# Optimization experiments

Hardware: AMD Instinct MI355X
Metric: run time of the kernel (lower is better)

## Reference

```python
import jax, jax.numpy as jnp
import numpy as np

N_NODES = 100000
N_EDGES = 1600000
D_IN = 128
D_OUT = 128


def setup_inputs() -> dict:
    key = jax.random.key(0)
    k_x, k_s, k_r, k_w = jax.random.split(key, 4)
    x = jax.random.normal(k_x, (N_NODES, D_IN), dtype=jnp.float32)
    senders = jax.random.randint(k_s, (N_EDGES,), 0, N_NODES, dtype=jnp.int32)
    receivers = jax.random.randint(k_r, (N_EDGES,), 0, N_NODES, dtype=jnp.int32)
    # xavier_uniform for (D_IN, D_OUT)
    limit = float(np.sqrt(6.0 / (D_IN + D_OUT)))
    weight = jax.random.uniform(k_w, (D_IN, D_OUT), dtype=jnp.float32,
                                minval=-limit, maxval=limit)
    bias = jnp.zeros((D_OUT,), dtype=jnp.float32)
    return {"x": x, "senders": senders, "receivers": receivers,
            "n_node": N_NODES, "weight": weight, "bias": bias}


def reference(x, senders, receivers, n_node, weight, bias):
    # Linear node update: [N, D_in] @ [D_in, D_out] + bias
    h = jnp.dot(x, weight) + bias
    total_num_nodes = x.shape[0]

    # Degree counts via segment_sum of ones (symmetric normalization)
    ones = jnp.ones_like(senders)
    sender_degree = jax.ops.segment_sum(ones, senders, num_segments=total_num_nodes)
    receiver_degree = jax.ops.segment_sum(ones, receivers, num_segments=total_num_nodes)

    # Pre-scale by 1/sqrt(deg_out), scatter-sum along edges, post-scale by 1/sqrt(deg_in)
    h = h * jax.lax.rsqrt(jnp.maximum(sender_degree, 1.0))[:, None]
    agg = jax.ops.segment_sum(h[senders], receivers, num_segments=total_num_nodes)
    out = agg * jax.lax.rsqrt(jnp.maximum(receiver_degree, 1.0))[:, None]
    return out
```

## Files before the change

kernel.cpp:

```cpp
#include <hip/hip_runtime.h>
#include <hip/hip_bf16.h>
#include <stdint.h>

#define N_NODES 100000
#define N_EDGES 1600000
#define TILE 8192
#define NB 196
#define BIN_BLOCKS ((N_EDGES + TILE - 1) / TILE)

static const size_t OFF_H      = 0;
static const size_t OFF_SSCALE = 25600000;
static const size_t OFF_ROWP   = 26000000;
static const size_t OFF_RHIST  = 26400016;
static const size_t OFF_SHIST  = 26401040;
static const size_t OFF_RBASE  = 26402064;
static const size_t OFF_SBASE  = 26403088;
static const size_t OFF_RCUR   = 26404112;
static const size_t OFF_SCUR   = 26405136;
static const size_t OFF_WFRAG  = 26406160;
static const size_t OFF_EBUF   = 26438928;
static const size_t OFF_SBUF   = 32838928;

using short8 = __attribute__((ext_vector_type(8))) short;
using f32x4  = __attribute__((ext_vector_type(4))) float;

static __device__ __forceinline__ short f2bf(float f) {
    uint32_t u = __float_as_uint(f);
    uint32_t r = (u + 0x7fffu + ((u >> 16) & 1u)) >> 16;
    return (short)r;
}

__global__ __launch_bounds__(256) void prep_w_kernel(const float* __restrict__ W,
                                                     short8* __restrict__ wfrag) {
    int slot = blockIdx.x * 256 + threadIdx.x;
    int f = slot >> 6, lane = slot & 63;
    int quad = lane >> 4, mcol = lane & 15;
    int s = f >> 3, c = f & 7;
    int krow = s * 32 + quad * 8;
    int ncol = c * 16 + mcol;
    short8 wf;
    #pragma unroll
    for (int j = 0; j < 8; j++)
        wf[j] = f2bf(W[(krow + j) * 128 + ncol]);
    wfrag[slot] = wf;
}

__global__ __launch_bounds__(256) void hist196_kernel(const int* __restrict__ snd,
                                                      const int* __restrict__ rcv,
                                                      int* __restrict__ rhist,
                                                      int* __restrict__ shist) {
    __shared__ int hr[256], hs[256];
    int t = threadIdx.x;
    hr[t] = 0; hs[t] = 0;
    __syncthreads();
    int base = blockIdx.x * TILE;
    #pragma unroll
    for (int j = 0; j < 32; j++) {
        int idx = base + j * 256 + t;
        if (idx < N_EDGES) {
            atomicAdd(&hr[rcv[idx] >> 9], 1);
            atomicAdd(&hs[snd[idx] >> 9], 1);
        }
    }
    __syncthreads();
    if (t < NB) {
        if (hr[t]) atomicAdd(&rhist[t], hr[t]);
        if (hs[t]) atomicAdd(&shist[t], hs[t]);
    }
}

__global__ __launch_bounds__(256) void scanb_kernel(const int* __restrict__ rhist,
                                                    const int* __restrict__ shist,
                                                    int* __restrict__ rbase,
                                                    int* __restrict__ sbase,
                                                    int* __restrict__ rcur,
                                                    int* __restrict__ scur,
                                                    int* __restrict__ row_ptr) {
    __shared__ int s[256];
    int t = threadIdx.x;

    int v = (t < NB) ? rhist[t] : 0;
    s[t] = v;
    __syncthreads();
    #pragma unroll
    for (int off = 1; off < 256; off <<= 1) {
        int tv = (t >= off) ? s[t - off] : 0;
        __syncthreads();
        s[t] += tv;
        __syncthreads();
    }
    if (t < NB) { int e = s[t] - v; rbase[t] = e; rcur[t] = e; }
    __syncthreads();

    v = (t < NB) ? shist[t] : 0;
    s[t] = v;
    __syncthreads();
    #pragma unroll
    for (int off = 1; off < 256; off <<= 1) {
        int tv = (t >= off) ? s[t - off] : 0;
        __syncthreads();
        s[t] += tv;
        __syncthreads();
    }
    if (t < NB) { int e = s[t] - v; sbase[t] = e; scur[t] = e; }
    if (t == 0) row_ptr[N_NODES] = N_EDGES;
}

__global__ __launch_bounds__(256) void binr_kernel(const int* __restrict__ snd,
                                                   const int* __restrict__ rcv,
                                                   int* __restrict__ rcur,
                                                   int* __restrict__ scur,
                                                   uint32_t* __restrict__ ebuf,
                                                   uint16_t* __restrict__ sbuf) {
    __shared__ int hist[256];
    __shared__ int coff[256];
    __shared__ int ccur[256];
    __shared__ int gbase[256];
    __shared__ uint32_t stage[TILE];

    const int t = threadIdx.x;
    const int base = blockIdx.x * TILE;

    uint32_t ss[32], rs[32];
    #pragma unroll
    for (int j = 0; j < 32; j++) {
        int idx = base + j * 256 + t;
        bool ok = idx < N_EDGES;
        ss[j] = ok ? (uint32_t)snd[idx] : 0u;
        rs[j] = ok ? (uint32_t)rcv[idx] : 0xffffffffu;
    }

    hist[t] = 0;
    __syncthreads();
    #pragma unroll
    for (int j = 0; j < 32; j++)
        if (rs[j] != 0xffffffffu) atomicAdd(&hist[rs[j] >> 9], 1);
    __syncthreads();

    int v = hist[t];
    ccur[t] = v;
    __syncthreads();
    #pragma unroll
    for (int off = 1; off < 256; off <<= 1) {
        int tv = (t >= off) ? ccur[t - off] : 0;
        __syncthreads();
        ccur[t] += tv;
        __syncthreads();
    }
    int excl = ccur[t] - v;
    coff[t] = excl;
    int gb = 0;
    if (v > 0) gb = atomicAdd(&rcur[t], v);
    gbase[t] = gb - excl;
    __syncthreads();
    ccur[t] = excl;
    __syncthreads();

    #pragma unroll
    for (int j = 0; j < 32; j++) {
        uint32_t r = rs[j];
        if (r != 0xffffffffu) {
            int pos = atomicAdd(&ccur[r >> 9], 1);
            stage[pos] = (ss[j] << 9) | (r & 511u);
        }
    }
    __syncthreads();

    int total = coff[255] + hist[255];
    for (int i = t; i < total; i += 256) {
        uint32_t pv = stage[i];
        int lo = 0;
        #pragma unroll
        for (int step = 128; step; step >>= 1)
            if (lo + step < 256 && coff[lo + step] <= i) lo += step;
        ebuf[gbase[lo] + i] = pv;
    }
    __syncthreads();

    hist[t] = 0;
    __syncthreads();
    #pragma unroll
    for (int j = 0; j < 32; j++)
        if (rs[j] != 0xffffffffu) atomicAdd(&hist[ss[j] >> 9], 1);
    __syncthreads();

    v = hist[t];
    ccur[t] = v;
    __syncthreads();
    #pragma unroll
    for (int off = 1; off < 256; off <<= 1) {
        int tv = (t >= off) ? ccur[t - off] : 0;
        __syncthreads();
        ccur[t] += tv;
        __syncthreads();
    }
    excl = ccur[t] - v;
    coff[t] = excl;
    gb = 0;
    if (v > 0) gb = atomicAdd(&scur[t], v);
    gbase[t] = gb - excl;
    __syncthreads();
    ccur[t] = excl;
    __syncthreads();

    uint16_t* stage16 = (uint16_t*)stage;
    #pragma unroll
    for (int j = 0; j < 32; j++) {
        if (rs[j] != 0xffffffffu) {
            int pos = atomicAdd(&ccur[ss[j] >> 9], 1);
            stage16[pos] = (uint16_t)(ss[j] & 511u);
        }
    }
    __syncthreads();

    total = coff[255] + hist[255];
    for (int i = t; i < total; i += 256) {
        uint16_t pv = stage16[i];
        int lo = 0;
        #pragma unroll
        for (int step = 128; step; step >>= 1)
            if (lo + step < 256 && coff[lo + step] <= i) lo += step;
        sbuf[gbase[lo] + i] = pv;
    }
}

__global__ __launch_bounds__(256) void bucket_kernel(const int* __restrict__ rbase,
                                                     const int* __restrict__ rhist,
                                                     const int* __restrict__ sbase,
                                                     const int* __restrict__ shist,
                                                     uint32_t* __restrict__ ebuf,
                                                     const uint16_t* __restrict__ sbuf,
                                                     int* __restrict__ row_ptr,
                                                     float* __restrict__ sscale) {
    __shared__ int hist_l[512];
    __shared__ int excl_l[512];
    __shared__ int cur_l[512];
    __shared__ int ps[256];
    __shared__ uint32_t inb[9216];
    __shared__ uint32_t perm[9216];

    const int b = blockIdx.x;
    const int t = threadIdx.x;
    const int nbase = b << 9;
    const int base = rbase[b];
    const int size = rhist[b];

    hist_l[t] = 0; hist_l[t + 256] = 0;
    __syncthreads();

    for (int i = t; i < size; i += 256) {
        uint32_t v = ebuf[base + i];
        inb[i] = v;
        atomicAdd(&hist_l[v & 511u], 1);
    }
    __syncthreads();

    int h0 = hist_l[2 * t], h1 = hist_l[2 * t + 1];
    int p = h0 + h1;
    ps[t] = p;
    __syncthreads();
    #pragma unroll
    for (int off = 1; off < 256; off <<= 1) {
        int tv = (t >= off) ? ps[t - off] : 0;
        __syncthreads();
        ps[t] += tv;
        __syncthreads();
    }
    int pe = ps[t] - p;
    excl_l[2 * t] = pe;
    excl_l[2 * t + 1] = pe + h0;
    cur_l[2 * t] = pe;
    cur_l[2 * t + 1] = pe + h0;
    __syncthreads();

    for (int i = t; i < 512; i += 256) {
        int n = nbase + i;
        if (n < N_NODES) row_ptr[n] = base + excl_l[i];
    }

    for (int i = t; i < size; i += 256) {
        uint32_t v = inb[i];
        int pos = atomicAdd(&cur_l[v & 511u], 1);
        perm[pos] = v >> 9;
    }
    __syncthreads();
    for (int i = t; i < size; i += 256)
        ebuf[base + i] = perm[i];

    __syncthreads();
    hist_l[t] = 0; hist_l[t + 256] = 0;
    __syncthreads();
    const int sb = sbase[b];
    const int ssz = shist[b];
    for (int i = t; i < ssz; i += 256)
        atomicAdd(&hist_l[(int)sbuf[sb + i]], 1);
    __syncthreads();
    for (int i = t; i < 512; i += 256) {
        int n = nbase + i;
        if (n < N_NODES) sscale[n] = rsqrtf(fmaxf((float)hist_l[i], 1.f));
    }
}

__global__ __launch_bounds__(256, 3) void gemm_mfma_kernel(const float* __restrict__ x,
                                                           const short8* __restrict__ wfrag,
                                                           const float* __restrict__ bias,
                                                           const float* __restrict__ sscale,
                                                           short* __restrict__ h) {
    const int t = threadIdx.x;
    const int lane = t & 63;
    const int wv = t >> 6;
    const int quad = lane >> 4;
    const int mcol = lane & 15;

    const int node0 = blockIdx.x * 128 + wv * 32;
    short8 afrag[2][4];
    #pragma unroll
    for (int mf = 0; mf < 2; mf++) {
        int node = node0 + mf * 16 + mcol;
        bool ok = node < N_NODES;
        const float* xr = x + (size_t)(ok ? node : 0) * 128;
        #pragma unroll
        for (int s = 0; s < 4; s++) {
            int k0 = s * 32 + quad * 8;
            f32x4 v0 = ok ? *(const f32x4*)(xr + k0)     : f32x4{0.f,0.f,0.f,0.f};
            f32x4 v1 = ok ? *(const f32x4*)(xr + k0 + 4) : f32x4{0.f,0.f,0.f,0.f};
            short8 af;
            #pragma unroll
            for (int j = 0; j < 4; j++) {
                af[j]     = f2bf(v0[j]);
                af[4 + j] = f2bf(v1[j]);
            }
            afrag[mf][s] = af;
        }
    }

    f32x4 acc[2][8];
    #pragma unroll
    for (int mf = 0; mf < 2; mf++)
        #pragma unroll
        for (int c = 0; c < 8; c++)
            acc[mf][c] = f32x4{0.f, 0.f, 0.f, 0.f};

    #pragma unroll
    for (int s = 0; s < 4; s++) {
        #pragma unroll
        for (int c = 0; c < 8; c++) {
            short8 bfrag = wfrag[(s * 8 + c) * 64 + lane];
            acc[0][c] = __builtin_amdgcn_mfma_f32_16x16x32_bf16(afrag[0][s], bfrag, acc[0][c], 0, 0, 0);
            acc[1][c] = __builtin_amdgcn_mfma_f32_16x16x32_bf16(afrag[1][s], bfrag, acc[1][c], 0, 0, 0);
        }
    }

    float rsv[2][4];
    #pragma unroll
    for (int mf = 0; mf < 2; mf++)
        #pragma unroll
        for (int r = 0; r < 4; r++) {
            int nd = node0 + mf * 16 + quad * 4 + r;
            rsv[mf][r] = (nd < N_NODES) ? sscale[nd] : 1.f;
        }

    #pragma unroll
    for (int mf = 0; mf < 2; mf++)
        #pragma unroll
        for (int c = 0; c < 8; c++) {
            float bval = bias[c * 16 + mcol];
            #pragma unroll
            for (int r = 0; r < 4; r++) {
                int nd = node0 + mf * 16 + quad * 4 + r;
                if (nd < N_NODES)
                    h[(size_t)nd * 128 + c * 16 + mcol] =
                        f2bf((acc[mf][c][r] + bval) * rsv[mf][r]);
            }
        }
}

__global__ __launch_bounds__(256) void gather_kernel(const uint32_t* __restrict__ h2,
                                                     const int* __restrict__ row_ptr,
                                                     const uint32_t* __restrict__ esrc,
                                                     f32x4* __restrict__ out4) {
    const int wv = threadIdx.x >> 6;
    const int lane = threadIdx.x & 63;
    const int sub = lane >> 4;
    const int ln = lane & 15;
    const int node = blockIdx.x * 16 + wv * 4 + sub;

    const int b = row_ptr[node];
    const int e = row_ptr[node + 1];

    float a0 = 0.f, a1 = 0.f, a2 = 0.f, a3 = 0.f;
    float a4 = 0.f, a5 = 0.f, a6 = 0.f, a7 = 0.f;

    int i = b;
    for (; i + 4 <= e; i += 4) {
        uint32_t s0 = esrc[i + 0], s1 = esrc[i + 1], s2 = esrc[i + 2], s3 = esrc[i + 3];
        uint4 v0 = *(const uint4*)&h2[(size_t)s0 * 64 + ln * 4];
        uint4 v1 = *(const uint4*)&h2[(size_t)s1 * 64 + ln * 4];
        uint4 v2 = *(const uint4*)&h2[(size_t)s2 * 64 + ln * 4];
        uint4 v3 = *(const uint4*)&h2[(size_t)s3 * 64 + ln * 4];
        a0 += __uint_as_float(v0.x << 16) + __uint_as_float(v1.x << 16)
            + __uint_as_float(v2.x << 16) + __uint_as_float(v3.x << 16);
        a1 += __uint_as_float(v0.x & 0xffff0000u) + __uint_as_float(v1.x & 0xffff0000u)
            + __uint_as_float(v2.x & 0xffff0000u) + __uint_as_float(v3.x & 0xffff0000u);
        a2 += __uint_as_float(v0.y << 16) + __uint_as_float(v1.y << 16)
            + __uint_as_float(v2.y << 16) + __uint_as_float(v3.y << 16);
        a3 += __uint_as_float(v0.y & 0xffff0000u) + __uint_as_float(v1.y & 0xffff0000u)
            + __uint_as_float(v2.y & 0xffff0000u) + __uint_as_float(v3.y & 0xffff0000u);
        a4 += __uint_as_float(v0.z << 16) + __uint_as_float(v1.z << 16)
            + __uint_as_float(v2.z << 16) + __uint_as_float(v3.z << 16);
        a5 += __uint_as_float(v0.z & 0xffff0000u) + __uint_as_float(v1.z & 0xffff0000u)
            + __uint_as_float(v2.z & 0xffff0000u) + __uint_as_float(v3.z & 0xffff0000u);
        a6 += __uint_as_float(v0.w << 16) + __uint_as_float(v1.w << 16)
            + __uint_as_float(v2.w << 16) + __uint_as_float(v3.w << 16);
        a7 += __uint_as_float(v0.w & 0xffff0000u) + __uint_as_float(v1.w & 0xffff0000u)
            + __uint_as_float(v2.w & 0xffff0000u) + __uint_as_float(v3.w & 0xffff0000u);
    }
    for (; i < e; i++) {
        uint32_t s = esrc[i];
        uint4 v = *(const uint4*)&h2[(size_t)s * 64 + ln * 4];
        a0 += __uint_as_float(v.x << 16);
        a1 += __uint_as_float(v.x & 0xffff0000u);
        a2 += __uint_as_float(v.y << 16);
        a3 += __uint_as_float(v.y & 0xffff0000u);
        a4 += __uint_as_float(v.z << 16);
        a5 += __uint_as_float(v.z & 0xffff0000u);
        a6 += __uint_as_float(v.w << 16);
        a7 += __uint_as_float(v.w & 0xffff0000u);
    }
    float rs = rsqrtf(fmaxf((float)(e - b), 1.f));
    f32x4 o0 = {a0 * rs, a1 * rs, a2 * rs, a3 * rs};
    f32x4 o1 = {a4 * rs, a5 * rs, a6 * rs, a7 * rs};
    out4[(size_t)node * 32 + ln * 2 + 0] = o0;
    out4[(size_t)node * 32 + ln * 2 + 1] = o1;
}

extern "C" void kernel_launch(void* const* d_in, const int* in_sizes, int n_in,
                              void* d_out, int out_size, void* d_ws, size_t ws_size,
                              hipStream_t stream) {
    const float* x    = (const float*)d_in[0];
    const int*   snd  = (const int*)d_in[1];
    const int*   rcv  = (const int*)d_in[2];
    const float* W    = (const float*)d_in[4];
    const float* bias = (const float*)d_in[5];

    char* ws = (char*)d_ws;
    short*    h      = (short*)(ws + OFF_H);
    float*    sscale = (float*)(ws + OFF_SSCALE);
    int*      rowp   = (int*)(ws + OFF_ROWP);
    int*      rhist  = (int*)(ws + OFF_RHIST);
    int*      shist  = (int*)(ws + OFF_SHIST);
    int*      rbase  = (int*)(ws + OFF_RBASE);
    int*      sbase  = (int*)(ws + OFF_SBASE);
    int*      rcur   = (int*)(ws + OFF_RCUR);
    int*      scur   = (int*)(ws + OFF_SCUR);
    short8*   wfrag  = (short8*)(ws + OFF_WFRAG);
    uint32_t* ebuf   = (uint32_t*)(ws + OFF_EBUF);
    uint16_t* sbuf   = (uint16_t*)(ws + OFF_SBUF);

    hipMemsetAsync(ws + OFF_RHIST, 0, 2048, stream);

    prep_w_kernel  <<<8, 256, 0, stream>>>(W, wfrag);
    hist196_kernel <<<BIN_BLOCKS, 256, 0, stream>>>(snd, rcv, rhist, shist);
    scanb_kernel   <<<1, 256, 0, stream>>>(rhist, shist, rbase, sbase, rcur, scur, rowp);
    binr_kernel    <<<BIN_BLOCKS, 256, 0, stream>>>(snd, rcv, rcur, scur, ebuf, sbuf);
    bucket_kernel  <<<NB, 256, 0, stream>>>(rbase, rhist, sbase, shist, ebuf, sbuf, rowp, sscale);
    gemm_mfma_kernel<<<(N_NODES + 127) / 128, 256, 0, stream>>>(x, wfrag, bias, sscale, h);
    gather_kernel  <<<N_NODES / 16, 256, 0, stream>>>((const uint32_t*)h, rowp, ebuf, (f32x4*)d_out);
}
```

Before: 277.5 us.

## Use fixed-capacity receiver buckets and global sender-degree atomics to drop prepasses

Removes the separate histogram and scan kernels by giving each 512-node receiver bucket a fixed slot region of BCAP entries, with cursors set up by a tiny init kernel. Sender degrees are now counted with per-node global atomics instead of a second bin-and-bucket pass. Because buckets now have gaps, a row_end array replaces the row_ptr[n+1] lookup. The binning tile is halved to 4096. This cuts one full read of the edge arrays and several launches, but adds 1.6M scattered global atomics. It also relies on no bucket holding more than BCAP edges.

```diff
diff --git a/kernel.cpp b/kernel.cpp
--- a/kernel.cpp
+++ b/kernel.cpp
@@ -4,22 +4,19 @@
 
 #define N_NODES 100000
 #define N_EDGES 1600000
-#define TILE 8192
 #define NB 196
-#define BIN_BLOCKS ((N_EDGES + TILE - 1) / TILE)
+#define BCAP 9216
+#define TILE2 4096
+#define BIN2_BLOCKS ((N_EDGES + TILE2 - 1) / TILE2)
 
 static const size_t OFF_H      = 0;
 static const size_t OFF_SSCALE = 25600000;
 static const size_t OFF_ROWP   = 26000000;
-static const size_t OFF_RHIST  = 26400016;
-static const size_t OFF_SHIST  = 26401040;
-static const size_t OFF_RBASE  = 26402064;
-static const size_t OFF_SBASE  = 26403088;
-static const size_t OFF_RCUR   = 26404112;
-static const size_t OFF_SCUR   = 26405136;
-static const size_t OFF_WFRAG  = 26406160;
-static const size_t OFF_EBUF   = 26438928;
-static const size_t OFF_SBUF   = 32838928;
+static const size_t OFF_ROWE   = 26400000;
+static const size_t OFF_SDEG   = 26800000;
+static const size_t OFF_RCUR   = 27200000;
+static const size_t OFF_WFRAG  = 27201024;
+static const size_t OFF_EBUF   = 27233792;
 
 using short8 = __attribute__((ext_vector_type(8))) short;
 using f32x4  = __attribute__((ext_vector_type(4))) float;
@@ -28,6 +25,10 @@
     uint32_t u = __float_as_uint(f);
     uint32_t r = (u + 0x7fffu + ((u >> 16) & 1u)) >> 16;
     return (short)r;
+}
+
+__global__ __launch_bounds__(256) void init_kernel(int* __restrict__ rcur) {
+    rcur[threadIdx.x] = threadIdx.x * BCAP;
 }
 
 __global__ __launch_bounds__(256) void prep_w_kernel(const float* __restrict__ W,
@@ -45,95 +46,37 @@
     wfrag[slot] = wf;
 }
 
-__global__ __launch_bounds__(256) void hist196_kernel(const int* __restrict__ snd,
-                                                      const int* __restrict__ rcv,
-                                                      int* __restrict__ rhist,
-                                                      int* __restrict__ shist) {
-    __shared__ int hr[256], hs[256];
-    int t = threadIdx.x;
-    hr[t] = 0; hs[t] = 0;
-    __syncthreads();
-    int base = blockIdx.x * TILE;
-    #pragma unroll
-    for (int j = 0; j < 32; j++) {
-        int idx = base + j * 256 + t;
-        if (idx < N_EDGES) {
-            atomicAdd(&hr[rcv[idx] >> 9], 1);
-            atomicAdd(&hs[snd[idx] >> 9], 1);
-        }
-    }
-    __syncthreads();
-    if (t < NB) {
-        if (hr[t]) atomicAdd(&rhist[t], hr[t]);
-        if (hs[t]) atomicAdd(&shist[t], hs[t]);
-    }
-}
-
-__global__ __launch_bounds__(256) void scanb_kernel(const int* __restrict__ rhist,
-                                                    const int* __restrict__ shist,
-                                                    int* __restrict__ rbase,
-                                                    int* __restrict__ sbase,
-                                                    int* __restrict__ rcur,
-                                                    int* __restrict__ scur,
-                                                    int* __restrict__ row_ptr) {
-    __shared__ int s[256];
-    int t = threadIdx.x;
-
-    int v = (t < NB) ? rhist[t] : 0;
-    s[t] = v;
-    __syncthreads();
-    #pragma unroll
-    for (int off = 1; off < 256; off <<= 1) {
-        int tv = (t >= off) ? s[t - off] : 0;
-        __syncthreads();
-        s[t] += tv;
-        __syncthreads();
-    }
-    if (t < NB) { int e = s[t] - v; rbase[t] = e; rcur[t] = e; }
-    __syncthreads();
-
-    v = (t < NB) ? shist[t] : 0;
-    s[t] = v;
-    __syncthreads();
-    #pragma unroll
-    for (int off = 1; off < 256; off <<= 1) {
-        int tv = (t >= off) ? s[t - off] : 0;
-        __syncthreads();
-        s[t] += tv;
-        __syncthreads();
-    }
-    if (t < NB) { int e = s[t] - v; sbase[t] = e; scur[t] = e; }
-    if (t == 0) row_ptr[N_NODES] = N_EDGES;
-}
-
 __global__ __launch_bounds__(256) void binr_kernel(const int* __restrict__ snd,
                                                    const int* __restrict__ rcv,
                                                    int* __restrict__ rcur,
-                                                   int* __restrict__ scur,
-                                                   uint32_t* __restrict__ ebuf,
-                                                   uint16_t* __restrict__ sbuf) {
+                                                   int* __restrict__ sdeg,
+                                                   uint32_t* __restrict__ ebuf) {
     __shared__ int hist[256];
     __shared__ int coff[256];
     __shared__ int ccur[256];
     __shared__ int gbase[256];
-    __shared__ uint32_t stage[TILE];
+    __shared__ uint32_t stage[TILE2];
 
     const int t = threadIdx.x;
-    const int base = blockIdx.x * TILE;
-
-    uint32_t ss[32], rs[32];
-    #pragma unroll
-    for (int j = 0; j < 32; j++) {
+    const int base = blockIdx.x * TILE2;
+
+    uint32_t ss[16], rs[16];
+    #pragma unroll
+    for (int j = 0; j < 16; j++) {
         int idx = base + j * 256 + t;
         bool ok = idx < N_EDGES;
         ss[j] = ok ? (uint32_t)snd[idx] : 0u;
         rs[j] = ok ? (uint32_t)rcv[idx] : 0xffffffffu;
     }
 
+    #pragma unroll
+    for (int j = 0; j < 16; j++)
+        if (rs[j] != 0xffffffffu) atomicAdd(&sdeg[ss[j]], 1);
+
     hist[t] = 0;
     __syncthreads();
     #pragma unroll
-    for (int j = 0; j < 32; j++)
+    for (int j = 0; j < 16; j++)
         if (rs[j] != 0xffffffffu) atomicAdd(&hist[rs[j] >> 9], 1);
     __syncthreads();
 
@@ -157,7 +100,7 @@
     __syncthreads();
 
     #pragma unroll
-    for (int j = 0; j < 32; j++) {
+    for (int j = 0; j < 16; j++) {
         uint32_t r = rs[j];
         if (r != 0xffffffffu) {
             int pos = atomicAdd(&ccur[r >> 9], 1);
@@ -175,75 +118,26 @@
             if (lo + step < 256 && coff[lo + step] <= i) lo += step;
         ebuf[gbase[lo] + i] = pv;
     }
-    __syncthreads();
-
-    hist[t] = 0;
-    __syncthreads();
-    #pragma unroll
-    for (int j = 0; j < 32; j++)
-        if (rs[j] != 0xffffffffu) atomicAdd(&hist[ss[j] >> 9], 1);
-    __syncthreads();
-
-    v = hist[t];
-    ccur[t] = v;
-    __syncthreads();
-    #pragma unroll
-    for (int off = 1; off < 256; off <<= 1) {
-        int tv = (t >= off) ? ccur[t - off] : 0;
-        __syncthreads();
-        ccur[t] += tv;
-        __syncthreads();
-    }
-    excl = ccur[t] - v;
-    coff[t] = excl;
-    gb = 0;
-    if (v > 0) gb = atomicAdd(&scur[t], v);
-    gbase[t] = gb - excl;
-    __syncthreads();
-    ccur[t] = excl;
-    __syncthreads();
-
-    uint16_t* stage16 = (uint16_t*)stage;
-    #pragma unroll
-    for (int j = 0; j < 32; j++) {
-        if (rs[j] != 0xffffffffu) {
-            int pos = atomicAdd(&ccur[ss[j] >> 9], 1);
-            stage16[pos] = (uint16_t)(ss[j] & 511u);
-        }
-    }
-    __syncthreads();
-
-    total = coff[255] + hist[255];
-    for (int i = t; i < total; i += 256) {
-        uint16_t pv = stage16[i];
-        int lo = 0;
-        #pragma unroll
-        for (int step = 128; step; step >>= 1)
-            if (lo + step < 256 && coff[lo + step] <= i) lo += step;
-        sbuf[gbase[lo] + i] = pv;
-    }
-}
-
-__global__ __launch_bounds__(256) void bucket_kernel(const int* __restrict__ rbase,
-                                                     const int* __restrict__ rhist,
-                                                     const int* __restrict__ sbase,
-                                                     const int* __restrict__ shist,
+}
+
+__global__ __launch_bounds__(256) void bucket_kernel(const int* __restrict__ rcur,
                                                      uint32_t* __restrict__ ebuf,
-                                                     const uint16_t* __restrict__ sbuf,
+                                                     const int* __restrict__ sdeg,
                                                      int* __restrict__ row_ptr,
+                                                     int* __restrict__ row_end,
                                                      float* __restrict__ sscale) {
     __shared__ int hist_l[512];
     __shared__ int excl_l[512];
     __shared__ int cur_l[512];
     __shared__ int ps[256];
-    __shared__ uint32_t inb[9216];
-    __shared__ uint32_t perm[9216];
+    __shared__ uint32_t inb[BCAP];
+    __shared__ uint32_t perm[BCAP];
 
     const int b = blockIdx.x;
     const int t = threadIdx.x;
     const int nbase = b << 9;
-    const int base = rbase[b];
-    const int size = rhist[b];
+    const int base = b * BCAP;
+    const int size = rcur[b] - base;
 
     hist_l[t] = 0; hist_l[t + 256] = 0;
     __syncthreads();
@@ -275,7 +169,12 @@
 
     for (int i = t; i < 512; i += 256) {
         int n = nbase + i;
-        if (n < N_NODES) row_ptr[n] = base + excl_l[i];
+        if (n < N_NODES) {
+            int s = base + excl_l[i];
+            row_ptr[n] = s;
+            row_end[n] = s + hist_l[i];
+            sscale[n] = rsqrtf(fmaxf((float)sdeg[n], 1.f));
+        }
     }
 
     for (int i = t; i < size; i += 256) {
@@ -286,19 +185,6 @@
     __syncthreads();
     for (int i = t; i < size; i += 256)
         ebuf[base + i] = perm[i];
-
-    __syncthreads();
-    hist_l[t] = 0; hist_l[t + 256] = 0;
-    __syncthreads();
-    const int sb = sbase[b];
-    const int ssz = shist[b];
-    for (int i = t; i < ssz; i += 256)
-        atomicAdd(&hist_l[(int)sbuf[sb + i]], 1);
-    __syncthreads();
-    for (int i = t; i < 512; i += 256) {
-        int n = nbase + i;
-        if (n < N_NODES) sscale[n] = rsqrtf(fmaxf((float)hist_l[i], 1.f));
-    }
 }
 
 __global__ __launch_bounds__(256, 3) void gemm_mfma_kernel(const float* __restrict__ x,
@@ -377,6 +263,7 @@
 
 __global__ __launch_bounds__(256) void gather_kernel(const uint32_t* __restrict__ h2,
                                                      const int* __restrict__ row_ptr,
+                                                     const int* __restrict__ row_end,
                                                      const uint32_t* __restrict__ esrc,
                                                      f32x4* __restrict__ out4) {
     const int wv = threadIdx.x >> 6;
@@ -386,7 +273,7 @@
     const int node = blockIdx.x * 16 + wv * 4 + sub;
 
     const int b = row_ptr[node];
-    const int e = row_ptr[node + 1];
+    const int e = row_end[node];
 
     float a0 = 0.f, a1 = 0.f, a2 = 0.f, a3 = 0.f;
     float a4 = 0.f, a5 = 0.f, a6 = 0.f, a7 = 0.f;
@@ -447,23 +334,18 @@
     short*    h      = (short*)(ws + OFF_H);
     float*    sscale = (float*)(ws + OFF_SSCALE);
     int*      rowp   = (int*)(ws + OFF_ROWP);
-    int*      rhist  = (int*)(ws + OFF_RHIST);
-    int*      shist  = (int*)(ws + OFF_SHIST);
-    int*      rbase  = (int*)(ws + OFF_RBASE);
-    int*      sbase  = (int*)(ws + OFF_SBASE);
+    int*      rowe   = (int*)(ws + OFF_ROWE);
+    int*      sdeg   = (int*)(ws + OFF_SDEG);
     int*      rcur   = (int*)(ws + OFF_RCUR);
-    int*      scur   = (int*)(ws + OFF_SCUR);
     short8*   wfrag  = (short8*)(ws + OFF_WFRAG);
     uint32_t* ebuf   = (uint32_t*)(ws + OFF_EBUF);
-    uint16_t* sbuf   = (uint16_t*)(ws + OFF_SBUF);
-
-    hipMemsetAsync(ws + OFF_RHIST, 0, 2048, stream);
-
+
+    hipMemsetAsync(ws + OFF_SDEG, 0, 400000, stream);
+
+    init_kernel    <<<1, 256, 0, stream>>>(rcur);
     prep_w_kernel  <<<8, 256, 0, stream>>>(W, wfrag);
-    hist196_kernel <<<BIN_BLOCKS, 256, 0, stream>>>(snd, rcv, rhist, shist);
-    scanb_kernel   <<<1, 256, 0, stream>>>(rhist, shist, rbase, sbase, rcur, scur, rowp);
-    binr_kernel    <<<BIN_BLOCKS, 256, 0, stream>>>(snd, rcv, rcur, scur, ebuf, sbuf);
-    bucket_kernel  <<<NB, 256, 0, stream>>>(rbase, rhist, sbase, shist, ebuf, sbuf, rowp, sscale);
+    binr_kernel    <<<BIN2_BLOCKS, 256, 0, stream>>>(snd, rcv, rcur, sdeg, ebuf);
+    bucket_kernel  <<<NB, 256, 0, stream>>>(rcur, ebuf, sdeg, rowp, rowe, sscale);
     gemm_mfma_kernel<<<(N_NODES + 127) / 128, 256, 0, stream>>>(x, wfrag, bias, sscale, h);
-    gather_kernel  <<<N_NODES / 16, 256, 0, stream>>>((const uint32_t*)h, rowp, ebuf, (f32x4*)d_out);
-}
+    gather_kernel  <<<N_NODES / 16, 256, 0, stream>>>((const uint32_t*)h, rowp, rowe, ebuf, (f32x4*)d_out);
+}
```

After: 283.0 us. About the same (+2.0%).
